# Performance work log

Hardware: AMD Instinct MI355X
Metric: run time of the kernel (lower is better)

The kernel has to match this reference:

```python
import jax, jax.numpy as jnp
import numpy as np

B, T, H = 2048, 200, 128
A0, A1 = 64, 16


def setup_inputs() -> dict:
    key = jax.random.key(0)
    ks = jax.random.split(key, 12)
    s = 0.05  # init scale (upstream uses tiny init_std; larger keeps dynamics non-trivial)
    d = {}
    d["query"] = jax.random.normal(ks[0], (B, 1, H), jnp.float32)
    d["keys"] = jax.random.normal(ks[1], (B, T, H), jnp.float32)
    d["W0"] = jax.random.normal(ks[2], (A0, 4 * H), jnp.float32) * s
    d["b0"] = jnp.zeros((A0,), jnp.float32)
    d["W1"] = jax.random.normal(ks[3], (A1, A0), jnp.float32) * s
    d["b1"] = jnp.zeros((A1,), jnp.float32)
    d["Wd"] = jax.random.normal(ks[4], (1, A1), jnp.float32) * s
    d["bd"] = jnp.zeros((1,), jnp.float32)
    d["Wih"] = jax.random.normal(ks[5], (3 * H, H), jnp.float32) * s
    d["Whh"] = jax.random.normal(ks[6], (3 * H, H), jnp.float32) * s
    d["bih"] = jnp.zeros((3 * H,), jnp.float32)
    d["bhh"] = jnp.zeros((3 * H,), jnp.float32)
    d["keys_length"] = jax.random.randint(ks[7], (B, 1), 1, T + 1, jnp.int32)
    return d


def _forward(query, keys, W0, b0, W1, b1, Wd, bd, Wih, Whh, bih, bhh, keys_length):
    b, t, h = keys.shape
    q = jnp.broadcast_to(query, (b, t, h))
    # DIN attention: concat [q, k, q-k, q*k] -> sigmoid MLP -> scalar score
    ai = jnp.concatenate([q, keys, q - keys, q * keys], axis=-1)  # [B,T,4H]
    a = jax.nn.sigmoid(jnp.einsum('bti,oi->bto', ai, W0) + b0)
    a = jax.nn.sigmoid(jnp.einsum('bti,oi->bto', a, W1) + b1)
    score = (jnp.einsum('bti,oi->bto', a, Wd) + bd)[..., 0]  # [B,T]
    valid = jnp.arange(t)[None, :] < keys_length  # [B,T] True at valid steps
    att = jnp.where(valid, score, 0.0)
    # AUGRU over packed (equiv. length-masked) sequence
    gi = jnp.einsum('bti,oi->bto', keys, Wih) + bih  # precomputed input transform [B,T,3H]

    def step(hprev, inp):
        gi_t, a_t, v_t = inp  # [B,3H], [B], [B]
        gh = hprev @ Whh.T + bhh
        i_r, i_z, i_n = jnp.split(gi_t, 3, axis=-1)
        h_r, h_z, h_n = jnp.split(gh, 3, axis=-1)
        r = jax.nn.sigmoid(i_r + h_r)
        z = jax.nn.sigmoid(i_z + h_z)
        n = jnp.tanh(i_n + r * h_n)
        z = a_t[:, None] * z  # attention-modulated update gate
        hnew = (1.0 - z) * hprev + z * n
        hnew = jnp.where(v_t[:, None], hnew, hprev)  # freeze past sequence end
        return hnew, None

    h0 = jnp.zeros((b, h), keys.dtype)
    hT, _ = jax.lax.scan(step, h0, (gi.transpose(1, 0, 2), att.T, valid.T))
    # rows with keys_length == 0 would be zero (here lengths >= 1)
    return hT * (keys_length > 0).astype(hT.dtype)


def reference(query, keys, W0, b0, W1, b1, Wd, bd, Wih, Whh, bih, bhh, keys_length):
    return _forward(query, keys, W0, b0, W1, b1, Wd, bd, Wih, Whh, bih, bhh, keys_length)
```

## Files before the change

### kernel.cpp

```cpp
#include <hip/hip_runtime.h>
#include <stdint.h>
#include <stddef.h>

#define B_N   2048
#define T_SEQ 200
#define H_DIM 128

typedef __attribute__((ext_vector_type(8))) short short8;
typedef __attribute__((ext_vector_type(4))) float floatx4;

#define OFF_ATT 0u
#define OFF_C   819200u
#define OFF_U1  1343488u
#define OFF_FR  1376256u
#define OFF_W1F 1409024u

__device__ __forceinline__ unsigned rnd_bf(float f) {
  union { float f; unsigned u; } v; v.f = f;
  return v.u + 0x7FFFu + ((v.u >> 16) & 1u);
}
__device__ __forceinline__ unsigned short f2bf(float f) {
  return (unsigned short)(rnd_bf(f) >> 16);
}
__device__ __forceinline__ unsigned pack2bf(float lo, float hi) {
  return __builtin_amdgcn_perm(rnd_bf(hi), rnd_bf(lo), 0x07060302u);
}
__device__ __forceinline__ float bf2f(unsigned short u) {
  union { unsigned u; float f; } v; v.u = ((unsigned)u) << 16; return v.f;
}

#define LOG2E 1.4426950408889634f
__device__ __forceinline__ float fsig(float x) {
  return __builtin_amdgcn_rcpf(1.0f + __builtin_amdgcn_exp2f(-LOG2E * x));
}
__device__ __forceinline__ float ftanh(float x) {
  return fmaf(2.0f, __builtin_amdgcn_rcpf(1.0f + __builtin_amdgcn_exp2f(-2.0f * LOG2E * x)), -1.0f);
}

__device__ __forceinline__ floatx4 mfma16(short8 a, short8 b, floatx4 c) {
  return __builtin_amdgcn_mfma_f32_16x16x32_bf16(a, b, c, 0, 0, 0);
}
__device__ __forceinline__ short8 pack8(const float* p) {
  short8 r;
#pragma unroll
  for (int j = 0; j < 8; ++j) r[j] = (short)f2bf(p[j]);
  return r;
}

__global__ __launch_bounds__(256) void prep_kernel(
    const float* __restrict__ W0, const float* __restrict__ W1,
    float* __restrict__ u1_ws, short8* __restrict__ fr_ws,
    short8* __restrict__ w1f_ws)
{
  const int gid = blockIdx.x * 256 + threadIdx.x;
  const int gs  = gridDim.x * 256;
  for (int i = gid; i < 128 * 64; i += gs) {
    int k = i >> 6, o = i & 63;
    u1_ws[i] = W0[o * 512 + k] + W0[o * 512 + 256 + k];
  }
  for (int f = gid; f < 4 * 8 * 64; f += gs) {
    int ln = f & 63, kc = (f >> 6) & 7, tt = f >> 9;
    int o = tt * 16 + (ln & 15);
    int k0 = kc * 32 + ((ln >> 4) * 8);
    short8 v;
#pragma unroll
    for (int j = 0; j < 8; ++j) {
      int ks = k0 + j;
      float x = (ks < 128) ? (W0[o * 512 + 128 + ks] - W0[o * 512 + 256 + ks])
                           : W0[o * 512 + 384 + (ks - 128)];
      v[j] = (short)f2bf(x);
    }
    fr_ws[f] = v;
  }
  for (int f = gid; f < 2 * 64; f += gs) {
    int ln = f & 63, kc = f >> 6;
    int n = ln & 15, k0 = kc * 32 + ((ln >> 4) * 8);
    short8 v;
#pragma unroll
    for (int j = 0; j < 8; ++j) v[j] = (short)f2bf(W1[n * 64 + k0 + j]);
    w1f_ws[f] = v;
  }
}

__global__ __launch_bounds__(256) void c_kernel(
    const float* __restrict__ query, const float* __restrict__ u1_ws,
    const float* __restrict__ b0, float* __restrict__ c_ws)
{
  const int blk = blockIdx.x, tid = threadIdx.x;
  __shared__ float qs[16 * 128];
  for (int i = tid; i < 512; i += 256)
    *(float4*)&qs[i * 4] = *(const float4*)(query + (size_t)blk * 2048 + i * 4);
  __syncthreads();
  const int o = tid & 63, bb = tid >> 6;
  float a0 = b0[o], a1 = a0, a2 = a0, a3 = a0;
  const float* qr = qs + bb * 512;
#pragma unroll 4
  for (int k = 0; k < 128; ++k) {
    float w = u1_ws[k * 64 + o];
    a0 = fmaf(qr[k], w, a0);
    a1 = fmaf(qr[128 + k], w, a1);
    a2 = fmaf(qr[256 + k], w, a2);
    a3 = fmaf(qr[384 + k], w, a3);
  }
  const int b = blk * 16 + bb * 4;
  c_ws[(b + 0) * 64 + o] = a0;
  c_ws[(b + 1) * 64 + o] = a1;
  c_ws[(b + 2) * 64 + o] = a2;
  c_ws[(b + 3) * 64 + o] = a3;
}

__global__ __launch_bounds__(256) void att_kernel(
    const float* __restrict__ query, const float* __restrict__ keys,
    const float* __restrict__ c_ws, const short8* __restrict__ fr_ws,
    const short8* __restrict__ w1f_ws, const float* __restrict__ b1,
    const float* __restrict__ Wd, const float* __restrict__ bd,
    const int* __restrict__ klen, unsigned short* __restrict__ attb)
{
  const int b   = blockIdx.y;
  const int tt0 = blockIdx.x * 64;
  const int tid = threadIdx.x;
  const int lane = tid & 63, wv = tid >> 6;
  const int kb = (lane >> 4) * 8;

  __shared__ float qs[H_DIM];
  __shared__ __align__(16) unsigned short A[64][264];
  __shared__ __align__(16) unsigned short a0b[64][72];
  __shared__ float a1s[64][20];

  const int len = klen[b];
  if (tt0 >= len) {
    for (int t2 = tid; t2 < 64; t2 += 256) {
      int tg = tt0 + t2;
      if (tg < T_SEQ) attb[(size_t)tg * B_N + b] = 0;
    }
    return;
  }

  if (tid < H_DIM) qs[tid] = query[(size_t)b * H_DIM + tid];
  __syncthreads();

  {
    int tl = tid >> 2, q4 = tid & 3;
    int tg = tt0 + tl;
    bool v = (tg < T_SEQ);
    const float* krow = keys + ((size_t)b * T_SEQ + (v ? tg : 0)) * H_DIM + q4 * 32;
#pragma unroll
    for (int i = 0; i < 32; i += 4) {
      float4 kv = v ? *(const float4*)(krow + i) : make_float4(0.f, 0.f, 0.f, 0.f);
      int col = q4 * 32 + i;
      *(unsigned*)&A[tl][col]     = pack2bf(kv.x, kv.y);
      *(unsigned*)&A[tl][col + 2] = pack2bf(kv.z, kv.w);
      *(unsigned*)&A[tl][128 + col]     = pack2bf(kv.x * qs[col + 0], kv.y * qs[col + 1]);
      *(unsigned*)&A[tl][128 + col + 2] = pack2bf(kv.z * qs[col + 2], kv.w * qs[col + 3]);
    }
  }
  short8 bf[8];
  {
    const short8* frp = fr_ws + (size_t)wv * 8 * 64;
#pragma unroll
    for (int kc = 0; kc < 8; ++kc) bf[kc] = frp[kc * 64 + lane];
  }
  const float co = c_ws[(size_t)b * 64 + wv * 16 + (lane & 15)];
  __syncthreads();

#pragma unroll
  for (int tt = 0; tt < 4; ++tt) {
    floatx4 acc = {co, co, co, co};
    int row = tt * 16 + (lane & 15);
#pragma unroll
    for (int kc = 0; kc < 8; ++kc)
      acc = mfma16(*(const short8*)&A[row][kc * 32 + kb], bf[kc], acc);
#pragma unroll
    for (int r = 0; r < 4; ++r)
      a0b[tt * 16 + (lane >> 4) * 4 + r][wv * 16 + (lane & 15)] = f2bf(fsig(acc[r]));
  }
  __syncthreads();

  {
    short8 w1f0 = w1f_ws[lane], w1f1 = w1f_ws[64 + lane];
    float b1v = b1[lane & 15];
    floatx4 acc1 = {b1v, b1v, b1v, b1v};
    int r2 = wv * 16 + (lane & 15);
    acc1 = mfma16(*(const short8*)&a0b[r2][kb],      w1f0, acc1);
    acc1 = mfma16(*(const short8*)&a0b[r2][32 + kb], w1f1, acc1);
#pragma unroll
    for (int r = 0; r < 4; ++r)
      a1s[wv * 16 + (lane >> 4) * 4 + r][lane & 15] = fsig(acc1[r]);
  }
  __syncthreads();

  if (tid < 64) {
    int tg = tt0 + tid;
    if (tg < T_SEQ) {
      float s = bd[0];
#pragma unroll
      for (int i = 0; i < 16; ++i) s += a1s[tid][i] * Wd[i];
      attb[(size_t)tg * B_N + b] = (tg < len) ? f2bf(s) : (unsigned short)0;
    }
  }
}

__global__ __launch_bounds__(512, 2) void scan_kernel(
    const float* __restrict__ keys, const float* __restrict__ Wih,
    const float* __restrict__ Whh, const float* __restrict__ bih,
    const float* __restrict__ bhh, const int* __restrict__ klen,
    const unsigned short* __restrict__ attb, float* __restrict__ out)
{
  const int r0 = blockIdx.x * 16;
  const int tid = threadIdx.x;
  const int lane = tid & 63, wv = tid >> 6;

  __shared__ __align__(16) unsigned short hbf[2][16][136];
  __shared__ __align__(16) unsigned short kbf[2][16][136];
  __shared__ __align__(16) float att_s[T_SEQ][16];
  __shared__ int len_s[16];

  if (tid < 16) len_s[tid] = klen[r0 + tid];
  for (int i = tid; i < 16 * 136; i += 512) ((unsigned short*)hbf[0])[i] = 0;
  for (int i = tid; i < T_SEQ * 16; i += 512) {
    int t = i >> 4, m = i & 15;
    att_s[t][m] = bf2f(attb[(size_t)t * B_N + r0 + m]);
  }
  const int pm = tid >> 5, pj = (tid & 31) * 4;
  const float* kbase = keys + ((size_t)(r0 + pm) * T_SEQ) * H_DIM + pj;
  {
    float4 k0 = *(const float4*)kbase;
    float4 k1 = *(const float4*)(kbase + H_DIM);
    uint2 p0; p0.x = pack2bf(k0.x, k0.y); p0.y = pack2bf(k0.z, k0.w);
    uint2 p1; p1.x = pack2bf(k1.x, k1.y); p1.y = pack2bf(k1.z, k1.w);
    *(uint2*)&kbf[0][pm][pj] = p0;
    *(uint2*)&kbf[1][pm][pj] = p1;
  }
  float4 kvA = *(const float4*)(kbase + 2 * H_DIM);
  float4 kvB;

  short8 whf[3][4], wif[3][4];
  const int ocol = wv * 16 + (lane & 15);
  const int kb = (lane >> 4) * 8;
#pragma unroll
  for (int g = 0; g < 3; ++g) {
    int row = g * 128 + ocol;
#pragma unroll
    for (int kc = 0; kc < 4; ++kc) {
      int kk = kc * 32 + kb;
      whf[g][kc] = pack8(Whh + (size_t)row * H_DIM + kk);
      wif[g][kc] = pack8(Wih + (size_t)row * H_DIM + kk);
    }
  }
  const float br_  = bih[ocol] + bhh[ocol];
  const float bz_  = bih[128 + ocol] + bhh[128 + ocol];
  const float bin_ = bih[256 + ocol];
  const float bhn_ = bhh[256 + ocol];

  int tmax = 0;
#pragma unroll
  for (int m = 0; m < 16; ++m) tmax = max(tmax, len_s[m]);
  const int mrow0 = (lane >> 4) * 4;
  int lenr[4];
  float hreg[4];
#pragma unroll
  for (int r = 0; r < 4; ++r) { lenr[r] = len_s[mrow0 + r]; hreg[r] = 0.0f; }
  const int arow = lane & 15;

  __syncthreads();
  short8 akA[4], akB[4];
  akA[0] = *(const short8*)&kbf[0][arow][kb];
  akA[1] = *(const short8*)&kbf[0][arow][32 + kb];
  akA[2] = *(const short8*)&kbf[0][arow][64 + kb];
  akA[3] = *(const short8*)&kbf[0][arow][96 + kb];
  __syncthreads();

#define SCAN_STEP(BUF, NB, AKC, AKN, KVC, KVN, TT)                              \
  do {                                                                          \
    short8 ah0 = *(const short8*)&hbf[BUF][arow][kb];                           \
    short8 ah1 = *(const short8*)&hbf[BUF][arow][32 + kb];                      \
    short8 ah2 = *(const short8*)&hbf[BUF][arow][64 + kb];                      \
    short8 ah3 = *(const short8*)&hbf[BUF][arow][96 + kb];                      \
    floatx4 att4 = *(const floatx4*)&att_s[TT][mrow0];                          \
    int tf = (TT) + 3; if (tf > T_SEQ - 1) tf = T_SEQ - 1;                      \
    KVN = *(const float4*)(kbase + (size_t)tf * H_DIM);                         \
                     \
    floatx4 ark = {0.f, 0.f, 0.f, 0.f};                                         \
    floatx4 azk = {0.f, 0.f, 0.f, 0.f};                                         \
    floatx4 ain = {bin_, bin_, bin_, bin_};                                     \
    ark = mfma16(AKC[0], wif[0][0], ark); ark = mfma16(AKC[1], wif[0][1], ark); \
    ark = mfma16(AKC[2], wif[0][2], ark); ark = mfma16(AKC[3], wif[0][3], ark); \
    azk = mfma16(AKC[0], wif[1][0], azk); azk = mfma16(AKC[1], wif[1][1], azk); \
    azk = mfma16(AKC[2], wif[1][2], azk); azk = mfma16(AKC[3], wif[1][3], azk); \
    ain = mfma16(AKC[0], wif[2][0], ain); ain = mfma16(AKC[1], wif[2][1], ain); \
    ain = mfma16(AKC[2], wif[2][2], ain); ain = mfma16(AKC[3], wif[2][3], ain); \
       \
    AKN[0] = *(const short8*)&kbf[NB][arow][kb];                                \
    AKN[1] = *(const short8*)&kbf[NB][arow][32 + kb];                           \
    AKN[2] = *(const short8*)&kbf[NB][arow][64 + kb];                           \
    AKN[3] = *(const short8*)&kbf[NB][arow][96 + kb];                           \
    {   \
      uint2 p; p.x = pack2bf(KVC.x, KVC.y); p.y = pack2bf(KVC.z, KVC.w);        \
      *(uint2*)&kbf[BUF][pm][pj] = p;                                           \
    }                                                                           \
                   \
    floatx4 arh = {br_, br_, br_, br_};                                         \
    floatx4 azh = {bz_, bz_, bz_, bz_};                                         \
    floatx4 ahn = {bhn_, bhn_, bhn_, bhn_};                                     \
    arh = mfma16(ah0, whf[0][0], arh); arh = mfma16(ah1, whf[0][1], arh);       \
    arh = mfma16(ah2, whf[0][2], arh); arh = mfma16(ah3, whf[0][3], arh);       \
    azh = mfma16(ah0, whf[1][0], azh); azh = mfma16(ah1, whf[1][1], azh);       \
    azh = mfma16(ah2, whf[1][2], azh); azh = mfma16(ah3, whf[1][3], azh);       \
    ahn = mfma16(ah0, whf[2][0], ahn); ahn = mfma16(ah1, whf[2][1], ahn);       \
    ahn = mfma16(ah2, whf[2][2], ahn); ahn = mfma16(ah3, whf[2][3], ahn);       \
    _Pragma("unroll")                                                           \
    for (int r = 0; r < 4; ++r) {                                               \
      float rr = fsig(arh[r] + ark[r]);                                         \
      float zz = fsig(azh[r] + azk[r]);                                         \
      float nn = ftanh(ain[r] + rr * ahn[r]);                                   \
      float z2 = att4[r] * zz;                                                  \
      float hn = fmaf(z2, nn - hreg[r], hreg[r]);                               \
      hreg[r] = ((TT) < lenr[r]) ? hn : hreg[r];                                \
      hbf[NB][mrow0 + r][ocol] = f2bf(hreg[r]);                                 \
    }                                                                           \
            \
    __asm__ volatile("s_waitcnt lgkmcnt(0)\n\ts_barrier" ::: "memory");         \
  } while (0)

  int t = 0;
  for (; t + 1 < tmax; t += 2) {
    SCAN_STEP(0, 1, akA, akB, kvA, kvB, t);
    SCAN_STEP(1, 0, akB, akA, kvB, kvA, t + 1);
  }
  if (t < tmax) SCAN_STEP(0, 1, akA, akB, kvA, kvB, t);
#undef SCAN_STEP

#pragma unroll
  for (int r = 0; r < 4; ++r)
    out[(size_t)(r0 + mrow0 + r) * H_DIM + ocol] = hreg[r];
}

extern "C" void kernel_launch(void* const* d_in, const int* in_sizes, int n_in,
                              void* d_out, int out_size, void* d_ws, size_t ws_size,
                              hipStream_t stream) {
  const float* query = (const float*)d_in[0];
  const float* keys  = (const float*)d_in[1];
  const float* W0    = (const float*)d_in[2];
  const float* b0    = (const float*)d_in[3];
  const float* W1    = (const float*)d_in[4];
  const float* b1    = (const float*)d_in[5];
  const float* Wd    = (const float*)d_in[6];
  const float* bd    = (const float*)d_in[7];
  const float* Wih   = (const float*)d_in[8];
  const float* Whh   = (const float*)d_in[9];
  const float* bih   = (const float*)d_in[10];
  const float* bhh   = (const float*)d_in[11];
  const int*   klen  = (const int*)d_in[12];

  char* ws = (char*)d_ws;
  unsigned short* att_bf = (unsigned short*)(ws + OFF_ATT);
  float*  c_ws  = (float*)(ws + OFF_C);
  float*  u1_ws = (float*)(ws + OFF_U1);
  short8* fr_ws = (short8*)(ws + OFF_FR);
  short8* w1f_ws = (short8*)(ws + OFF_W1F);
  float* out = (float*)d_out;

  hipLaunchKernelGGL(prep_kernel, dim3(8), dim3(256), 0, stream, W0, W1, u1_ws, fr_ws, w1f_ws);
  hipLaunchKernelGGL(c_kernel, dim3(B_N / 16), dim3(256), 0, stream, query, u1_ws, b0, c_ws);
  hipLaunchKernelGGL(att_kernel, dim3(4, B_N), dim3(256), 0, stream,
                     query, keys, c_ws, fr_ws, w1f_ws, b1, Wd, bd, klen, att_bf);
  hipLaunchKernelGGL(scan_kernel, dim3(B_N / 16), dim3(512), 0, stream,
                     keys, Wih, Whh, bih, bhh, klen, att_bf, out);
}
```

Baseline: 526.8 us.

## Fold sigmoid/tanh scales into GRU weights, drop length mask, restructure att kernel

```diff
diff --git a/kernel.cpp b/kernel.cpp
--- a/kernel.cpp
+++ b/kernel.cpp
@@ -33,17 +33,14 @@
 __device__ __forceinline__ float fsig(float x) {
   return __builtin_amdgcn_rcpf(1.0f + __builtin_amdgcn_exp2f(-LOG2E * x));
 }
-__device__ __forceinline__ float ftanh(float x) {
-  return fmaf(2.0f, __builtin_amdgcn_rcpf(1.0f + __builtin_amdgcn_exp2f(-2.0f * LOG2E * x)), -1.0f);
-}
 
 __device__ __forceinline__ floatx4 mfma16(short8 a, short8 b, floatx4 c) {
   return __builtin_amdgcn_mfma_f32_16x16x32_bf16(a, b, c, 0, 0, 0);
 }
-__device__ __forceinline__ short8 pack8(const float* p) {
+__device__ __forceinline__ short8 pack8s(const float* p, float s) {
   short8 r;
 #pragma unroll
-  for (int j = 0; j < 8; ++j) r[j] = (short)f2bf(p[j]);
+  for (int j = 0; j < 8; ++j) r[j] = (short)f2bf(p[j] * s);
   return r;
 }
 
@@ -116,8 +113,7 @@
     const float* __restrict__ Wd, const float* __restrict__ bd,
     const int* __restrict__ klen, unsigned short* __restrict__ attb)
 {
-  const int b   = blockIdx.y;
-  const int tt0 = blockIdx.x * 64;
+  const int b   = blockIdx.x;
   const int tid = threadIdx.x;
   const int lane = tid & 63, wv = tid >> 6;
   const int kb = (lane >> 4) * 8;
@@ -128,76 +124,79 @@
   __shared__ float a1s[64][20];
 
   const int len = klen[b];
-  if (tt0 >= len) {
-    for (int t2 = tid; t2 < 64; t2 += 256) {
-      int tg = tt0 + t2;
-      if (tg < T_SEQ) attb[(size_t)tg * B_N + b] = 0;
-    }
-    return;
-  }
 
   if (tid < H_DIM) qs[tid] = query[(size_t)b * H_DIM + tid];
-  __syncthreads();
-
-  {
-    int tl = tid >> 2, q4 = tid & 3;
-    int tg = tt0 + tl;
-    bool v = (tg < T_SEQ);
-    const float* krow = keys + ((size_t)b * T_SEQ + (v ? tg : 0)) * H_DIM + q4 * 32;
-#pragma unroll
-    for (int i = 0; i < 32; i += 4) {
-      float4 kv = v ? *(const float4*)(krow + i) : make_float4(0.f, 0.f, 0.f, 0.f);
-      int col = q4 * 32 + i;
-      *(unsigned*)&A[tl][col]     = pack2bf(kv.x, kv.y);
-      *(unsigned*)&A[tl][col + 2] = pack2bf(kv.z, kv.w);
-      *(unsigned*)&A[tl][128 + col]     = pack2bf(kv.x * qs[col + 0], kv.y * qs[col + 1]);
-      *(unsigned*)&A[tl][128 + col + 2] = pack2bf(kv.z * qs[col + 2], kv.w * qs[col + 3]);
-    }
-  }
+
   short8 bf[8];
   {
     const short8* frp = fr_ws + (size_t)wv * 8 * 64;
 #pragma unroll
     for (int kc = 0; kc < 8; ++kc) bf[kc] = frp[kc * 64 + lane];
   }
+  short8 w1f0 = w1f_ws[lane], w1f1 = w1f_ws[64 + lane];
+  const float b1v = b1[lane & 15];
   const float co = c_ws[(size_t)b * 64 + wv * 16 + (lane & 15)];
+  const float bd0 = bd[0];
+  float wd_r[16];
+#pragma unroll
+  for (int i = 0; i < 16; ++i) wd_r[i] = Wd[i];
   __syncthreads();
 
-#pragma unroll
-  for (int tt = 0; tt < 4; ++tt) {
-    floatx4 acc = {co, co, co, co};
-    int row = tt * 16 + (lane & 15);
-#pragma unroll
-    for (int kc = 0; kc < 8; ++kc)
-      acc = mfma16(*(const short8*)&A[row][kc * 32 + kb], bf[kc], acc);
-#pragma unroll
-    for (int r = 0; r < 4; ++r)
-      a0b[tt * 16 + (lane >> 4) * 4 + r][wv * 16 + (lane & 15)] = f2bf(fsig(acc[r]));
-  }
-  __syncthreads();
-
-  {
-    short8 w1f0 = w1f_ws[lane], w1f1 = w1f_ws[64 + lane];
-    float b1v = b1[lane & 15];
-    floatx4 acc1 = {b1v, b1v, b1v, b1v};
-    int r2 = wv * 16 + (lane & 15);
-    acc1 = mfma16(*(const short8*)&a0b[r2][kb],      w1f0, acc1);
-    acc1 = mfma16(*(const short8*)&a0b[r2][32 + kb], w1f1, acc1);
-#pragma unroll
-    for (int r = 0; r < 4; ++r)
-      a1s[wv * 16 + (lane >> 4) * 4 + r][lane & 15] = fsig(acc1[r]);
-  }
-  __syncthreads();
-
-  if (tid < 64) {
-    int tg = tt0 + tid;
-    if (tg < T_SEQ) {
-      float s = bd[0];
-#pragma unroll
-      for (int i = 0; i < 16; ++i) s += a1s[tid][i] * Wd[i];
-      attb[(size_t)tg * B_N + b] = (tg < len) ? f2bf(s) : (unsigned short)0;
-    }
-  }
+  int t0 = 0;
+  for (; t0 < len; t0 += 64) {
+    {
+      int tl = tid >> 2, q4 = tid & 3;
+      int tg = t0 + tl;
+      bool v = (tg < T_SEQ);
+      const float* krow = keys + ((size_t)b * T_SEQ + (v ? tg : 0)) * H_DIM + q4 * 32;
+#pragma unroll
+      for (int i = 0; i < 32; i += 4) {
+        float4 kv = v ? *(const float4*)(krow + i) : make_float4(0.f, 0.f, 0.f, 0.f);
+        int col = q4 * 32 + i;
+        *(unsigned*)&A[tl][col]     = pack2bf(kv.x, kv.y);
+        *(unsigned*)&A[tl][col + 2] = pack2bf(kv.z, kv.w);
+        *(unsigned*)&A[tl][128 + col]     = pack2bf(kv.x * qs[col + 0], kv.y * qs[col + 1]);
+        *(unsigned*)&A[tl][128 + col + 2] = pack2bf(kv.z * qs[col + 2], kv.w * qs[col + 3]);
+      }
+    }
+    __syncthreads();
+
+#pragma unroll
+    for (int tt = 0; tt < 4; ++tt) {
+      floatx4 acc = {co, co, co, co};
+      int row = tt * 16 + (lane & 15);
+#pragma unroll
+      for (int kc = 0; kc < 8; ++kc)
+        acc = mfma16(*(const short8*)&A[row][kc * 32 + kb], bf[kc], acc);
+#pragma unroll
+      for (int r = 0; r < 4; ++r)
+        a0b[tt * 16 + (lane >> 4) * 4 + r][wv * 16 + (lane & 15)] = f2bf(fsig(acc[r]));
+    }
+    __syncthreads();
+
+    {
+      floatx4 acc1 = {b1v, b1v, b1v, b1v};
+      int r2 = wv * 16 + (lane & 15);
+      acc1 = mfma16(*(const short8*)&a0b[r2][kb],      w1f0, acc1);
+      acc1 = mfma16(*(const short8*)&a0b[r2][32 + kb], w1f1, acc1);
+#pragma unroll
+      for (int r = 0; r < 4; ++r)
+        a1s[wv * 16 + (lane >> 4) * 4 + r][lane & 15] = fsig(acc1[r]);
+    }
+    __syncthreads();
+
+    if (tid < 64) {
+      int tg = t0 + tid;
+      if (tg < T_SEQ) {
+        float s = bd0;
+#pragma unroll
+        for (int i = 0; i < 16; ++i) s += a1s[tid][i] * wd_r[i];
+        attb[(size_t)b * T_SEQ + tg] = (tg < len) ? f2bf(s) : (unsigned short)0;
+      }
+    }
+    __syncthreads();
+  }
+  for (int i = t0 + tid; i < T_SEQ; i += 256) attb[(size_t)b * T_SEQ + i] = 0;
 }
 
 __global__ __launch_bounds__(512, 2) void scan_kernel(
@@ -217,9 +216,14 @@
 
   if (tid < 16) len_s[tid] = klen[r0 + tid];
   for (int i = tid; i < 16 * 136; i += 512) ((unsigned short*)hbf[0])[i] = 0;
-  for (int i = tid; i < T_SEQ * 16; i += 512) {
-    int t = i >> 4, m = i & 15;
-    att_s[t][m] = bf2f(attb[(size_t)t * B_N + r0 + m]);
+  {
+    const unsigned* attw = (const unsigned*)attb;
+    for (int i = tid; i < 16 * 100; i += 512) {
+      int m = i / 100, t2 = i - m * 100;
+      unsigned w = attw[(size_t)(r0 + m) * 100 + t2];
+      att_s[2 * t2][m]     = bf2f((unsigned short)(w & 0xFFFFu));
+      att_s[2 * t2 + 1][m] = bf2f((unsigned short)(w >> 16));
+    }
   }
   const int pm = tid >> 5, pj = (tid & 31) * 4;
   const float* kbase = keys + ((size_t)(r0 + pm) * T_SEQ) * H_DIM + pj;
@@ -239,27 +243,27 @@
   const int kb = (lane >> 4) * 8;
 #pragma unroll
   for (int g = 0; g < 3; ++g) {
+    const float sc = (g == 2) ? (-2.0f * LOG2E) : (-LOG2E);
     int row = g * 128 + ocol;
 #pragma unroll
     for (int kc = 0; kc < 4; ++kc) {
       int kk = kc * 32 + kb;
-      whf[g][kc] = pack8(Whh + (size_t)row * H_DIM + kk);
-      wif[g][kc] = pack8(Wih + (size_t)row * H_DIM + kk);
-    }
-  }
-  const float br_  = bih[ocol] + bhh[ocol];
-  const float bz_  = bih[128 + ocol] + bhh[128 + ocol];
-  const float bin_ = bih[256 + ocol];
-  const float bhn_ = bhh[256 + ocol];
+      whf[g][kc] = pack8s(Whh + (size_t)row * H_DIM + kk, sc);
+      wif[g][kc] = pack8s(Wih + (size_t)row * H_DIM + kk, sc);
+    }
+  }
+  const float br_  = -LOG2E * (bih[ocol] + bhh[ocol]);
+  const float bz_  = -LOG2E * (bih[128 + ocol] + bhh[128 + ocol]);
+  const float bin_ = -2.0f * LOG2E * bih[256 + ocol];
+  const float bhn_ = -2.0f * LOG2E * bhh[256 + ocol];
 
   int tmax = 0;
 #pragma unroll
   for (int m = 0; m < 16; ++m) tmax = max(tmax, len_s[m]);
   const int mrow0 = (lane >> 4) * 4;
-  int lenr[4];
   float hreg[4];
 #pragma unroll
-  for (int r = 0; r < 4; ++r) { lenr[r] = len_s[mrow0 + r]; hreg[r] = 0.0f; }
+  for (int r = 0; r < 4; ++r) hreg[r] = 0.0f;
   const int arow = lane & 15;
 
   __syncthreads();
@@ -310,12 +314,12 @@
     ahn = mfma16(ah2, whf[2][2], ahn); ahn = mfma16(ah3, whf[2][3], ahn);       \
     _Pragma("unroll")                                                           \
     for (int r = 0; r < 4; ++r) {                                               \
-      float rr = fsig(arh[r] + ark[r]);                                         \
-      float zz = fsig(azh[r] + azk[r]);                                         \
-      float nn = ftanh(ain[r] + rr * ahn[r]);                                   \
+      float rr = __builtin_amdgcn_rcpf(1.0f + __builtin_amdgcn_exp2f(arh[r] + ark[r])); \
+      float zz = __builtin_amdgcn_rcpf(1.0f + __builtin_amdgcn_exp2f(azh[r] + azk[r])); \
+      float sn = fmaf(rr, ahn[r], ain[r]);                                      \
+      float nn = fmaf(2.0f, __builtin_amdgcn_rcpf(1.0f + __builtin_amdgcn_exp2f(sn)), -1.0f); \
       float z2 = att4[r] * zz;                                                  \
-      float hn = fmaf(z2, nn - hreg[r], hreg[r]);                               \
-      hreg[r] = ((TT) < lenr[r]) ? hn : hreg[r];                                \
+      hreg[r] = fmaf(z2, nn - hreg[r], hreg[r]);                                \
       hbf[NB][mrow0 + r][ocol] = f2bf(hreg[r]);                                 \
     }                                                                           \
             \
@@ -362,7 +366,7 @@
 
   hipLaunchKernelGGL(prep_kernel, dim3(8), dim3(256), 0, stream, W0, W1, u1_ws, fr_ws, w1f_ws);
   hipLaunchKernelGGL(c_kernel, dim3(B_N / 16), dim3(256), 0, stream, query, u1_ws, b0, c_ws);
-  hipLaunchKernelGGL(att_kernel, dim3(4, B_N), dim3(256), 0, stream,
+  hipLaunchKernelGGL(att_kernel, dim3(B_N), dim3(256), 0, stream,
                      query, keys, c_ws, fr_ws, w1f_ws, b1, Wd, bd, klen, att_bf);
   hipLaunchKernelGGL(scan_kernel, dim3(B_N / 16), dim3(512), 0, stream,
                      keys, Wih, Whh, bih, bhh, klen, att_bf, out);
```

After: 477.4 us. 1.1x faster.
